# Optimization experiments

Hardware: AMD Instinct MI355X
Metric: run time of the kernel (lower is better)

Reference implementation:

```python
import jax, jax.numpy as jnp
import numpy as np
import math
from itertools import combinations_with_replacement

M_MODES = 10      # photonic modes
N_PHOT = 5        # photons in input state [1,0,1,0,...]
HIDDEN = 100      # number of px phase shifters (hidden_dim)
IN_DIM = 784
N_CLASSES = 10
BATCH = 128

# Fock output states with bunching: multisets of N_PHOT modes -> C(14,5)=2002
_STATES = np.array(list(combinations_with_replacement(range(M_MODES), N_PHOT)), dtype=np.int32)  # [S, n] row indices
_FACT = np.array([
    np.prod([math.factorial(int(c)) for c in np.bincount(s, minlength=M_MODES)])
    for s in _STATES
], dtype=np.float32)  # prod t_j! per output state
# Input-state mode columns (occupied modes) and factorial product (=1 since all occupancies are 1)
_IN_COLS = np.array([0, 2, 4, 6, 8], dtype=np.int32)
# Ryser subsets over n=5 rows
_BITS = np.array([[(k >> i) & 1 for i in range(N_PHOT)] for k in range(2 ** N_PHOT)], dtype=np.float32)  # [K, n]
_SIGNS = ((-1.0) ** (N_PHOT - _BITS.sum(axis=1))).astype(np.float32)  # (-1)^n * (-1)^{|S|}


def _rand_unitary(rng, m):
    z = rng.standard_normal((m, m)) + 1j * rng.standard_normal((m, m))
    q, r = np.linalg.qr(z)
    q = q * (np.diag(r) / np.abs(np.diag(r)))
    return q.astype(np.complex64)


def setup_inputs() -> dict:
    rng = np.random.default_rng(0)
    x = jnp.asarray(rng.standard_normal((BATCH, IN_DIM)), dtype=jnp.float32)
    W1 = jnp.asarray(rng.standard_normal((HIDDEN, IN_DIM)) * 0.03, dtype=jnp.float32)
    b1 = jnp.zeros((HIDDEN,), dtype=jnp.float32)
    UL = _rand_unitary(rng, M_MODES)
    UR = _rand_unitary(rng, M_MODES)
    S = _STATES.shape[0]
    W2 = jnp.asarray(rng.standard_normal((N_CLASSES, S)) * 0.02, dtype=jnp.float32)
    b2 = jnp.zeros((N_CLASSES,), dtype=jnp.float32)
    return {
        "x": x, "W1": W1, "b1": b1,
        "wl_re": jnp.asarray(UL.real), "wl_im": jnp.asarray(UL.imag),
        "wr_re": jnp.asarray(UR.real), "wr_im": jnp.asarray(UR.imag),
        "W2": W2, "b2": b2,
    }


def _forward(x, W1, b1, wl_re, wl_im, wr_re, wr_im, W2, b2):
    B = x.shape[0]
    # downscaling linear + sigmoid -> phase-shifter values px in (0,1)
    h = jax.nn.sigmoid(x @ W1.T + b1)  # [B, HIDDEN]
    # phase shifter i sits on mode i % m; commuting phases on a mode sum
    theta = h.reshape(B, HIDDEN // M_MODES, M_MODES).sum(axis=1)  # [B, m]
    WL = (wl_re + 1j * wl_im).astype(jnp.complex64)
    WR = (wr_re + 1j * wr_im).astype(jnp.complex64)
    phase = jnp.exp(1j * theta.astype(jnp.complex64))  # [B, m]
    # total unitary U = WR @ diag(phase) @ WL
    U = jnp.einsum('pq,bq,qr->bpr', WR, phase, WL)  # [B, m, m]
    A = U[:, :, _IN_COLS]  # columns for occupied input modes -> [B, m, n]
    # per output Fock state, take rows (with multiplicity) -> [B, S, n, n]
    Mx = A[:, jnp.asarray(_STATES), :]
    masks = jnp.asarray(_BITS)   # [K, n]
    signs = jnp.asarray(_SIGNS)  # [K]
    # Ryser: perm = (-1)^n sum_S (-1)^{|S|} prod_j (sum_{i in S} M[i,j])
    rs = jnp.einsum('kn,bsnj->bskj', masks, Mx)       # [B, S, K, n]
    p = jnp.prod(rs, axis=-1)                          # [B, S, K]
    perm = jnp.einsum('k,bsk->bs', signs, p)           # [B, S] complex
    amp = perm / jnp.sqrt(jnp.asarray(_FACT))
    prob = amp.real ** 2 + amp.imag ** 2               # boson-sampling output distribution [B, S]
    return prob @ W2.T + b2                            # output Linear [B, N_CLASSES]


def reference(x, W1, b1, wl_re, wl_im, wr_re, wr_im, W2, b2):
    return _forward(x, W1, b1, wl_re, wl_im, wr_re, wr_im, W2, b2)
```

## Files before the change

kernel.cpp:

```cpp
#include <hip/hip_runtime.h>
#include <utility>
#include <math.h>

#define BATCH     128
#define IN_DIM    784
#define HIDDEN    100
#define MM        10
#define NPH       5
#define NSTATES   2002
#define NCLASSES  10

struct StateTbl { unsigned v[NSTATES]; };

constexpr StateTbl make_state_tbl() {
    StateTbl t{};
    int idx = 0;
    for (int a = 0; a < MM; ++a)
    for (int b = a; b < MM; ++b)
    for (int c = b; c < MM; ++c)
    for (int d = c; d < MM; ++d)
    for (int e = d; e < MM; ++e) {
        int cnt[MM] = {};
        cnt[a]++; cnt[b]++; cnt[c]++; cnt[d]++; cnt[e]++;
        int f = 1;
        for (int m = 0; m < MM; ++m) {
            int kf = 1;
            for (int i = 2; i <= cnt[m]; ++i) kf *= i;
            f *= kf;
        }
        t.v[idx++] = (unsigned)a | ((unsigned)b << 4) | ((unsigned)c << 8) |
                     ((unsigned)d << 12) | ((unsigned)e << 16) |
                     ((unsigned)f << 20);
    }
    return t;
}

__device__ const StateTbl STATE_TBL = make_state_tbl();

__global__ __launch_bounds__(256) void qc_stageA(
    const float* __restrict__ x, const float* __restrict__ W1,
    const float* __restrict__ b1,
    const float* __restrict__ wl_re, const float* __restrict__ wl_im,
    const float* __restrict__ wr_re, const float* __restrict__ wr_im,
    const float* __restrict__ b2,
    float* __restrict__ A_ws, float* __restrict__ out)
{
    __shared__ __align__(16) float xs[IN_DIM];
    __shared__ float part[200];
    __shared__ float hs[HIDDEN];
    __shared__ float phc[MM], phs_[MM];
    __shared__ float plr[50], pli[50];

    const int b   = blockIdx.x;
    const int tid = threadIdx.x;

    for (int i = tid; i < IN_DIM; i += 256) xs[i] = x[b * IN_DIM + i];
    if (tid < NCLASSES) out[b * NCLASSES + tid] = b2[tid];
    __syncthreads();

    if (tid < 200) {
        const int j = tid >> 1, half = tid & 1;
        const float* wr_ = W1 + j * IN_DIM + half * 392;
        const float* xr  = xs + half * 392;
        float4 acc = make_float4(0.f, 0.f, 0.f, 0.f);
        #pragma unroll 4
        for (int i = 0; i < 392; i += 4) {
            float4 w  = *(const float4*)(wr_ + i);
            float4 xv = *(const float4*)(xr + i);
            acc.x += w.x * xv.x; acc.y += w.y * xv.y;
            acc.z += w.z * xv.z; acc.w += w.w * xv.w;
        }
        part[tid] = (acc.x + acc.y) + (acc.z + acc.w);
    }
    __syncthreads();

    if (tid < HIDDEN) {
        float t = part[2 * tid] + part[2 * tid + 1] + b1[tid];
        hs[tid] = 1.0f / (1.0f + expf(-t));
    }
    __syncthreads();

    if (tid < MM) {
        float th = 0.f;
        #pragma unroll
        for (int g = 0; g < MM; ++g) th += hs[g * MM + tid];
        float sv, cv;
        sincosf(th, &sv, &cv);
        phc[tid] = cv; phs_[tid] = sv;
    }
    __syncthreads();

    if (tid < 50) {
        const int q = tid / 5, c = tid % 5;
        const float lr = wl_re[q * MM + 2 * c], li = wl_im[q * MM + 2 * c];
        plr[tid] = phc[q] * lr - phs_[q] * li;
        pli[tid] = phc[q] * li + phs_[q] * lr;
    }
    __syncthreads();

    if (tid < 50) {
        const int p = tid / 5, c = tid % 5;
        float ar = 0.f, ai = 0.f;
        #pragma unroll
        for (int q = 0; q < MM; ++q) {
            const float rr = wr_re[p * MM + q], ri = wr_im[p * MM + q];
            const float br = plr[q * 5 + c],    bi = pli[q * 5 + c];
            ar += rr * br - ri * bi;
            ai += rr * bi + ri * br;
        }
        A_ws[(b * 50 + tid) * 2 + 0] = ar;
        A_ws[(b * 50 + tid) * 2 + 1] = ai;
    }
}

template <int K>
__device__ __forceinline__ void glynn_step(
    const float (&mr)[5][5], const float (&mi)[5][5],
    float (&cr)[5], float (&ci)[5], float& accr, float& acci)
{
    constexpr int   bit  = (K & 1) ? 0 : ((K & 2) ? 1 : ((K & 4) ? 2 : 3));
    constexpr int   gray = K ^ (K >> 1);
    constexpr int   row  = bit + 1;
    constexpr float s2   = ((gray >> bit) & 1) ? -2.0f : 2.0f;
    constexpr int   pc   = (gray & 1) + ((gray >> 1) & 1) +
                           ((gray >> 2) & 1) + ((gray >> 3) & 1);
    #pragma unroll
    for (int j = 0; j < 5; ++j) {
        cr[j] = fmaf(s2, mr[row][j], cr[j]);
        ci[j] = fmaf(s2, mi[row][j], ci[j]);
    }
    float pr = cr[0], pi = ci[0];
    #pragma unroll
    for (int j = 1; j < 5; ++j) {
        const float nr = pr * cr[j] - pi * ci[j];
        const float ni = pr * ci[j] + pi * cr[j];
        pr = nr; pi = ni;
    }
    if constexpr ((pc & 1) != 0) { accr -= pr; acci -= pi; }
    else                         { accr += pr; acci += pi; }
}

template <int... Ks>
__device__ __forceinline__ void glynn_run(
    std::integer_sequence<int, Ks...>,
    const float (&mr)[5][5], const float (&mi)[5][5],
    float (&cr)[5], float (&ci)[5], float& accr, float& acci)
{
    (glynn_step<Ks + 1>(mr, mi, cr, ci, accr, acci), ...);
}

__global__ __launch_bounds__(256) void qc_stageB(
    const float* __restrict__ A_ws, const float* __restrict__ W2,
    float* __restrict__ out)
{
    __shared__ float2 a2[50];
    __shared__ float  wsum[4][NCLASSES];

    const int tid   = threadIdx.x;
    const int b     = blockIdx.x >> 2;
    const int sbase = (blockIdx.x & 3) << 9;

    if (tid < 50) a2[tid] = ((const float2*)A_ws)[b * 50 + tid];
    __syncthreads();

    float cls[NCLASSES] = {0,0,0,0,0,0,0,0,0,0};

    #pragma unroll
    for (int t = 0; t < 2; ++t) {
        const int s = sbase + (t << 8) + tid;
        if (s < NSTATES) {
            const unsigned w = STATE_TBL.v[s];

            float mr[5][5], mi[5][5];
            #pragma unroll
            for (int n = 0; n < 5; ++n) {
                const int base = ((w >> (4 * n)) & 15) * 5;
                #pragma unroll
                for (int j = 0; j < 5; ++j) {
                    const float2 e = a2[base + j];
                    mr[n][j] = e.x; mi[n][j] = e.y;
                }
            }

            float cr[5], ci[5];
            #pragma unroll
            for (int j = 0; j < 5; ++j) {
                cr[j] = ((mr[0][j] + mr[1][j]) + (mr[2][j] + mr[3][j])) + mr[4][j];
                ci[j] = ((mi[0][j] + mi[1][j]) + (mi[2][j] + mi[3][j])) + mi[4][j];
            }
            float accr = 0.f, acci = 0.f;
            {
                float pr = cr[0], pi = ci[0];
                #pragma unroll
                for (int j = 1; j < 5; ++j) {
                    const float nr = pr * cr[j] - pi * ci[j];
                    const float ni = pr * ci[j] + pi * cr[j];
                    pr = nr; pi = ni;
                }
                accr = pr; acci = pi;
            }
            glynn_run(std::make_integer_sequence<int, 15>{}, mr, mi, cr, ci, accr, acci);

            const float fact = (float)(w >> 20);
            const float prob = (accr * accr + acci * acci) / (256.0f * fact);

            #pragma unroll
            for (int c = 0; c < NCLASSES; ++c)
                cls[c] = fmaf(prob, W2[c * NSTATES + s], cls[c]);
        }
    }

    #pragma unroll
    for (int c = 0; c < NCLASSES; ++c) {
        float v = cls[c];
        #pragma unroll
        for (int off = 32; off > 0; off >>= 1) v += __shfl_down(v, off, 64);
        if ((tid & 63) == 0) wsum[tid >> 6][c] = v;
    }
    __syncthreads();
    if (tid < NCLASSES) {
        const float t = (wsum[0][tid] + wsum[1][tid]) + (wsum[2][tid] + wsum[3][tid]);
        atomicAdd(out + b * NCLASSES + tid, t);
    }
}

extern "C" void kernel_launch(void* const* d_in, const int* in_sizes, int n_in,
                              void* d_out, int out_size, void* d_ws, size_t ws_size,
                              hipStream_t stream)
{
    const float* x     = (const float*)d_in[0];
    const float* W1    = (const float*)d_in[1];
    const float* b1    = (const float*)d_in[2];
    const float* wl_re = (const float*)d_in[3];
    const float* wl_im = (const float*)d_in[4];
    const float* wr_re = (const float*)d_in[5];
    const float* wr_im = (const float*)d_in[6];
    const float* W2    = (const float*)d_in[7];
    const float* b2    = (const float*)d_in[8];
    float*       out   = (float*)d_out;
    float*       A_ws  = (float*)d_ws;

    qc_stageA<<<BATCH, 256, 0, stream>>>(x, W1, b1, wl_re, wl_im,
                                         wr_re, wr_im, b2, A_ws, out);
    qc_stageB<<<BATCH * 4, 256, 0, stream>>>(A_ws, W2, out);
}
```

Baseline: 95.47 us.

## Fuse phase-unitary stage and permanent stage into one kernel per batch row

Merges the two kernels into a single 512-thread block per batch element. The A matrix stays in shared memory instead of a global workspace, and the atomic accumulation and bias pre-init are replaced by a direct store. The W1 dot product is split four ways instead of two. This removes a launch and a global round-trip, but cuts the grid from 512 to 128 blocks, leaving many CUs idle during the permanent computation.

```diff
diff --git a/kernel.cpp b/kernel.cpp
--- a/kernel.cpp
+++ b/kernel.cpp
@@ -37,82 +37,6 @@
 
 __device__ const StateTbl STATE_TBL = make_state_tbl();
 
-__global__ __launch_bounds__(256) void qc_stageA(
-    const float* __restrict__ x, const float* __restrict__ W1,
-    const float* __restrict__ b1,
-    const float* __restrict__ wl_re, const float* __restrict__ wl_im,
-    const float* __restrict__ wr_re, const float* __restrict__ wr_im,
-    const float* __restrict__ b2,
-    float* __restrict__ A_ws, float* __restrict__ out)
-{
-    __shared__ __align__(16) float xs[IN_DIM];
-    __shared__ float part[200];
-    __shared__ float hs[HIDDEN];
-    __shared__ float phc[MM], phs_[MM];
-    __shared__ float plr[50], pli[50];
-
-    const int b   = blockIdx.x;
-    const int tid = threadIdx.x;
-
-    for (int i = tid; i < IN_DIM; i += 256) xs[i] = x[b * IN_DIM + i];
-    if (tid < NCLASSES) out[b * NCLASSES + tid] = b2[tid];
-    __syncthreads();
-
-    if (tid < 200) {
-        const int j = tid >> 1, half = tid & 1;
-        const float* wr_ = W1 + j * IN_DIM + half * 392;
-        const float* xr  = xs + half * 392;
-        float4 acc = make_float4(0.f, 0.f, 0.f, 0.f);
-        #pragma unroll 4
-        for (int i = 0; i < 392; i += 4) {
-            float4 w  = *(const float4*)(wr_ + i);
-            float4 xv = *(const float4*)(xr + i);
-            acc.x += w.x * xv.x; acc.y += w.y * xv.y;
-            acc.z += w.z * xv.z; acc.w += w.w * xv.w;
-        }
-        part[tid] = (acc.x + acc.y) + (acc.z + acc.w);
-    }
-    __syncthreads();
-
-    if (tid < HIDDEN) {
-        float t = part[2 * tid] + part[2 * tid + 1] + b1[tid];
-        hs[tid] = 1.0f / (1.0f + expf(-t));
-    }
-    __syncthreads();
-
-    if (tid < MM) {
-        float th = 0.f;
-        #pragma unroll
-        for (int g = 0; g < MM; ++g) th += hs[g * MM + tid];
-        float sv, cv;
-        sincosf(th, &sv, &cv);
-        phc[tid] = cv; phs_[tid] = sv;
-    }
-    __syncthreads();
-
-    if (tid < 50) {
-        const int q = tid / 5, c = tid % 5;
-        const float lr = wl_re[q * MM + 2 * c], li = wl_im[q * MM + 2 * c];
-        plr[tid] = phc[q] * lr - phs_[q] * li;
-        pli[tid] = phc[q] * li + phs_[q] * lr;
-    }
-    __syncthreads();
-
-    if (tid < 50) {
-        const int p = tid / 5, c = tid % 5;
-        float ar = 0.f, ai = 0.f;
-        #pragma unroll
-        for (int q = 0; q < MM; ++q) {
-            const float rr = wr_re[p * MM + q], ri = wr_im[p * MM + q];
-            const float br = plr[q * 5 + c],    bi = pli[q * 5 + c];
-            ar += rr * br - ri * bi;
-            ai += rr * bi + ri * br;
-        }
-        A_ws[(b * 50 + tid) * 2 + 0] = ar;
-        A_ws[(b * 50 + tid) * 2 + 1] = ai;
-    }
-}
-
 template <int K>
 __device__ __forceinline__ void glynn_step(
     const float (&mr)[5][5], const float (&mi)[5][5],
@@ -149,25 +73,88 @@
     (glynn_step<Ks + 1>(mr, mi, cr, ci, accr, acci), ...);
 }
 
-__global__ __launch_bounds__(256) void qc_stageB(
-    const float* __restrict__ A_ws, const float* __restrict__ W2,
+__global__ __launch_bounds__(512) void qc_fused(
+    const float* __restrict__ x, const float* __restrict__ W1,
+    const float* __restrict__ b1,
+    const float* __restrict__ wl_re, const float* __restrict__ wl_im,
+    const float* __restrict__ wr_re, const float* __restrict__ wr_im,
+    const float* __restrict__ W2, const float* __restrict__ b2,
     float* __restrict__ out)
 {
+    __shared__ __align__(16) float xs[IN_DIM];
+    __shared__ float  part[400];
+    __shared__ float  hs[HIDDEN];
+    __shared__ float  phc[MM], phs_[MM];
+    __shared__ float  plr[50], pli[50];
     __shared__ float2 a2[50];
-    __shared__ float  wsum[4][NCLASSES];
-
-    const int tid   = threadIdx.x;
-    const int b     = blockIdx.x >> 2;
-    const int sbase = (blockIdx.x & 3) << 9;
-
-    if (tid < 50) a2[tid] = ((const float2*)A_ws)[b * 50 + tid];
+    __shared__ float  wsum[8][NCLASSES];
+
+    const int b   = blockIdx.x;
+    const int tid = threadIdx.x;
+
+    for (int i = tid; i < IN_DIM; i += 512) xs[i] = x[b * IN_DIM + i];
+    __syncthreads();
+
+    if (tid < 400) {
+        const int j = tid >> 2, q = tid & 3;
+        const float* wr_ = W1 + j * IN_DIM + q * 196;
+        const float* xr  = xs + q * 196;
+        float4 acc = make_float4(0.f, 0.f, 0.f, 0.f);
+        #pragma unroll 7
+        for (int i = 0; i < 196; i += 4) {
+            float4 w  = *(const float4*)(wr_ + i);
+            float4 xv = *(const float4*)(xr + i);
+            acc.x += w.x * xv.x; acc.y += w.y * xv.y;
+            acc.z += w.z * xv.z; acc.w += w.w * xv.w;
+        }
+        part[tid] = (acc.x + acc.y) + (acc.z + acc.w);
+    }
+    __syncthreads();
+
+    if (tid < HIDDEN) {
+        float t = (part[4 * tid] + part[4 * tid + 1]) +
+                  (part[4 * tid + 2] + part[4 * tid + 3]) + b1[tid];
+        hs[tid] = 1.0f / (1.0f + expf(-t));
+    }
+    __syncthreads();
+
+    if (tid < MM) {
+        float th = 0.f;
+        #pragma unroll
+        for (int g = 0; g < MM; ++g) th += hs[g * MM + tid];
+        float sv, cv;
+        sincosf(th, &sv, &cv);
+        phc[tid] = cv; phs_[tid] = sv;
+    }
+    __syncthreads();
+
+    if (tid < 50) {
+        const int q = tid / 5, c = tid % 5;
+        const float lr = wl_re[q * MM + 2 * c], li = wl_im[q * MM + 2 * c];
+        plr[tid] = phc[q] * lr - phs_[q] * li;
+        pli[tid] = phc[q] * li + phs_[q] * lr;
+    }
+    __syncthreads();
+
+    if (tid < 50) {
+        const int p = tid / 5, c = tid % 5;
+        float ar = 0.f, ai = 0.f;
+        #pragma unroll
+        for (int q = 0; q < MM; ++q) {
+            const float rr = wr_re[p * MM + q], ri = wr_im[p * MM + q];
+            const float br = plr[q * 5 + c],    bi = pli[q * 5 + c];
+            ar += rr * br - ri * bi;
+            ai += rr * bi + ri * br;
+        }
+        a2[tid] = make_float2(ar, ai);
+    }
     __syncthreads();
 
     float cls[NCLASSES] = {0,0,0,0,0,0,0,0,0,0};
 
     #pragma unroll
-    for (int t = 0; t < 2; ++t) {
-        const int s = sbase + (t << 8) + tid;
+    for (int t = 0; t < 4; ++t) {
+        const int s = (t << 9) + tid;
         if (s < NSTATES) {
             const unsigned w = STATE_TBL.v[s];
 
@@ -188,7 +175,7 @@
                 cr[j] = ((mr[0][j] + mr[1][j]) + (mr[2][j] + mr[3][j])) + mr[4][j];
                 ci[j] = ((mi[0][j] + mi[1][j]) + (mi[2][j] + mi[3][j])) + mi[4][j];
             }
-            float accr = 0.f, acci = 0.f;
+            float accr, acci;
             {
                 float pr = cr[0], pi = ci[0];
                 #pragma unroll
@@ -219,8 +206,10 @@
     }
     __syncthreads();
     if (tid < NCLASSES) {
-        const float t = (wsum[0][tid] + wsum[1][tid]) + (wsum[2][tid] + wsum[3][tid]);
-        atomicAdd(out + b * NCLASSES + tid, t);
+        float t = 0.f;
+        #pragma unroll
+        for (int wv = 0; wv < 8; ++wv) t += wsum[wv][tid];
+        out[b * NCLASSES + tid] = t + b2[tid];
     }
 }
 
@@ -238,9 +227,7 @@
     const float* W2    = (const float*)d_in[7];
     const float* b2    = (const float*)d_in[8];
     float*       out   = (float*)d_out;
-    float*       A_ws  = (float*)d_ws;
-
-    qc_stageA<<<BATCH, 256, 0, stream>>>(x, W1, b1, wl_re, wl_im,
-                                         wr_re, wr_im, b2, A_ws, out);
-    qc_stageB<<<BATCH * 4, 256, 0, stream>>>(A_ws, W2, out);
-}
+
+    qc_fused<<<BATCH, 512, 0, stream>>>(x, W1, b1, wl_re, wl_im,
+                                        wr_re, wr_im, W2, b2, out);
+}
```

Result: faster. 87.47 us (-8.4%).
